# Performance work log

Hardware: AMD Instinct MI355X
Metric: run time of the kernel (lower is better)

The kernel has to match this reference:

```python
import jax, jax.numpy as jnp
import numpy as np

KERNEL_SIZE = 9
B, C, H, W = 8, 32, 512, 512


def setup_inputs() -> dict:
    key = jax.random.key(0)
    image = jax.random.uniform(key, (B, C, H, W), dtype=jnp.float32)
    return {"image": image}


def _make_kernels(channels, k, dtype):
    # kernel1: point-select (identity) depthwise kernel
    k1 = jnp.zeros((channels, 1, k, k), dtype=dtype).at[:, 0, k // 2, k // 2].set(1.0)
    # kernel2: all -2, center = k*k - 2
    k2 = jnp.full((channels, 1, k, k), -2.0, dtype=dtype).at[:, 0, k // 2, k // 2].set(float(k * k - 2))
    # kernel3: ones box filter
    k3 = jnp.ones((channels, 1, k, k), dtype=dtype)
    return k1, k2, k3


def _dwconv(x, ker, channels, k):
    pad = k // 2  # 'same' padding for odd k
    return jax.lax.conv_general_dilated(
        x, ker,
        window_strides=(1, 1),
        padding=[(pad, pad), (pad, pad)],
        dimension_numbers=("NCHW", "OIHW", "NCHW"),
        feature_group_count=channels,
    )


def reference(image):
    channels = image.shape[1]
    k = KERNEL_SIZE
    k1, k2, k3 = _make_kernels(channels, k, image.dtype)
    im_sq = jnp.square(image)
    conv1 = _dwconv(image, k1, channels, k)   # identity point-select
    conv2 = _dwconv(image, k2, channels, k)   # box(-2) with center correction
    conv3 = _dwconv(im_sq, k3, channels, k)   # box sum of squares
    convsum = conv1 * conv2 + conv3
    # sum over (C,H,W) per batch element, then mean over batch
    return jnp.mean(jnp.sum(convsum, axis=(1, 2, 3)))
```

## Files before the change

kernel.cpp:

```cpp
#include <hip/hip_runtime.h>

#define HH 512
#define WW 512
#define SEGS 16
#define SEGROWS 32
#define CG 128

__device__ __forceinline__ int imax(int a, int b) { return a > b ? a : b; }
__device__ __forceinline__ int imin(int a, int b) { return a < b ? a : b; }

__global__ __launch_bounds__(256, 4) void scc_kernel(const float* __restrict__ img,
                                                     float* __restrict__ out) {
    const int tid   = blockIdx.x * 256 + threadIdx.x;
    const int g     = tid & (CG - 1);
    const int rest  = tid >> 7;
    const int seg   = rest & (SEGS - 1);
    const int plane = rest >> 4;

    const float* base = img + (size_t)plane * (HH * WW);
    const int r0 = seg * SEGROWS;

    float4 cw;
    {
        int w0 = 4 * g;
        cw.x = (float)(9 - imax(0, 4 - (w0 + 0)) - imax(0, (w0 + 0) - (WW - 5)));
        cw.y = (float)(9 - imax(0, 4 - (w0 + 1)) - imax(0, (w0 + 1) - (WW - 5)));
        cw.z = (float)(9 - imax(0, 4 - (w0 + 2)) - imax(0, (w0 + 2) - (WW - 5)));
        cw.w = (float)(9 - imax(0, 4 - (w0 + 3)) - imax(0, (w0 + 3) - (WW - 5)));
    }

    const int offL = imax(g - 1, 0) * 16;
    const int offC = g * 16;
    const int offR = imin(g + 1, CG - 1) * 16;
    const float mL = (g > 0) ? 1.f : 0.f;
    const float mR = (g < CG - 1) ? 1.f : 0.f;

    const float4 z4 = make_float4(0.f, 0.f, 0.f, 0.f);
    float4 x0 = z4, x1 = z4, x2 = z4, x3 = z4, x4 = z4,
           x5 = z4, x6 = z4, x7 = z4, x8 = z4;
    float4 q0 = z4, q1 = z4, q2 = z4, q3 = z4, q4 = z4;
    float4 V = z4;
    float accW = 0.f, accRV = 0.f;

#pragma unroll 8
    for (int i = 0; i < SEGROWS + 8; ++i) {
        const int r  = r0 - 4 + i;
        const int rc_ = imin(imax(r, 0), HH - 1);
        const float m = ((unsigned)r < (unsigned)HH) ? 1.f : 0.f;
        const char* rowb = (const char*)(base + (ptrdiff_t)rc_ * WW);

        float4 lcr = *(const float4*)(rowb + offL);
        float4 ccr = *(const float4*)(rowb + offC);
        float4 rcr = *(const float4*)(rowb + offR);

        const float a = mL * m, b = mR * m;
        float4 lc = make_float4(lcr.x * a, lcr.y * a, lcr.z * a, lcr.w * a);
        float4 cc = make_float4(ccr.x * m, ccr.y * m, ccr.z * m, ccr.w * m);
        float4 rc = make_float4(rcr.x * b, rcr.y * b, rcr.z * b, rcr.w * b);

        float R0 = ((lc.x + lc.y) + (lc.z + lc.w)) + ((cc.x + cc.y) + (cc.z + cc.w)) + rc.x;
        float R1 = R0 - lc.x + rc.y;
        float R2 = R1 - lc.y + rc.z;
        float R3 = R2 - lc.z + rc.w;
        float4 Rn = make_float4(R0, R1, R2, R3);

        V.x += cc.x - x0.x;  V.y += cc.y - x0.y;
        V.z += cc.z - x0.z;  V.w += cc.w - x0.w;

        x0 = x1; x1 = x2; x2 = x3; x3 = x4; x4 = x5;
        x5 = x6; x6 = x7; x7 = x8; x8 = cc;
        q0 = q1; q1 = q2; q2 = q3; q3 = q4; q4 = Rn;

        if (i >= 8) {
            const int h = r - 4;
            const float chf = (float)(9 - imax(0, 4 - h) - imax(0, h - (HH - 5)));
            float w0 = fmaf(chf, cw.x, 81.f);
            float w1 = fmaf(chf, cw.y, 81.f);
            float w2 = fmaf(chf, cw.z, 81.f);
            float w3 = fmaf(chf, cw.w, 81.f);
            accW = fmaf(w0 * x4.x, x4.x, accW);
            accW = fmaf(w1 * x4.y, x4.y, accW);
            accW = fmaf(w2 * x4.z, x4.z, accW);
            accW = fmaf(w3 * x4.w, x4.w, accW);
            accRV = fmaf(q0.x, V.x, accRV);
            accRV = fmaf(q0.y, V.y, accRV);
            accRV = fmaf(q0.z, V.z, accRV);
            accRV = fmaf(q0.w, V.w, accRV);
        }
    }

    float acc = accW - 2.f * accRV;

#pragma unroll
    for (int off = 32; off > 0; off >>= 1)
        acc += __shfl_xor(acc, off, 64);
    __shared__ float wsum[4];
    const int lane = threadIdx.x & 63;
    const int wv   = threadIdx.x >> 6;
    if (lane == 0) wsum[wv] = acc;
    __syncthreads();
    if (threadIdx.x == 0) {
        float s = (wsum[0] + wsum[1]) + (wsum[2] + wsum[3]);
        atomicAdd(out, 0.125f * s);
    }
}

extern "C" void kernel_launch(void* const* d_in, const int* in_sizes, int n_in,
                              void* d_out, int out_size, void* d_ws, size_t ws_size,
                              hipStream_t stream) {
    const float* img = (const float*)d_in[0];
    float* out = (float*)d_out;
    hipMemsetAsync(out, 0, sizeof(float), stream);
    scc_kernel<<<dim3(2048), dim3(256), 0, stream>>>(img, out);
}
```

Baseline: 370.6 us.

## Replace register row history with cache reloads and peel warm-up loop

The nine-row float4 register history used for the vertical sliding sum is removed. The row leaving the window and the center row are now reloaded from memory, expected to hit in cache. The first eight warm-up rows are peeled into their own loop, which drops the per-iteration branch, and the launch-bounds occupancy hint is removed. This lowers register pressure and may improve occupancy, at the cost of two extra float4 loads per row.

```diff
diff --git a/kernel.cpp b/kernel.cpp
--- a/kernel.cpp
+++ b/kernel.cpp
@@ -9,8 +9,8 @@
 __device__ __forceinline__ int imax(int a, int b) { return a > b ? a : b; }
 __device__ __forceinline__ int imin(int a, int b) { return a < b ? a : b; }
 
-__global__ __launch_bounds__(256, 4) void scc_kernel(const float* __restrict__ img,
-                                                     float* __restrict__ out) {
+__global__ __launch_bounds__(256) void scc_kernel(const float* __restrict__ img,
+                                                  float* __restrict__ out) {
     const int tid   = blockIdx.x * 256 + threadIdx.x;
     const int g     = tid & (CG - 1);
     const int rest  = tid >> 7;
@@ -36,57 +36,76 @@
     const float mR = (g < CG - 1) ? 1.f : 0.f;
 
     const float4 z4 = make_float4(0.f, 0.f, 0.f, 0.f);
-    float4 x0 = z4, x1 = z4, x2 = z4, x3 = z4, x4 = z4,
-           x5 = z4, x6 = z4, x7 = z4, x8 = z4;
     float4 q0 = z4, q1 = z4, q2 = z4, q3 = z4, q4 = z4;
     float4 V = z4;
     float accW = 0.f, accRV = 0.f;
 
-#pragma unroll 8
-    for (int i = 0; i < SEGROWS + 8; ++i) {
-        const int r  = r0 - 4 + i;
-        const int rc_ = imin(imax(r, 0), HH - 1);
-        const float m = ((unsigned)r < (unsigned)HH) ? 1.f : 0.f;
-        const char* rowb = (const char*)(base + (ptrdiff_t)rc_ * WW);
+#pragma unroll
+    for (int i = 0; i < 8; ++i) {
+        const int r   = r0 - 4 + i;
+        const int rcl = imax(r, 0);
+        const float m = (r >= 0) ? 1.f : 0.f;
+        const char* rowb = (const char*)(base + (ptrdiff_t)rcl * WW);
+        float4 L = *(const float4*)(rowb + offL);
+        float4 C = *(const float4*)(rowb + offC);
+        float4 Rv = *(const float4*)(rowb + offR);
+        const float a = mL * m, b = mR * m;
+        float4 lc = make_float4(L.x * a, L.y * a, L.z * a, L.w * a);
+        float4 cc = make_float4(C.x * m, C.y * m, C.z * m, C.w * m);
+        float4 rc = make_float4(Rv.x * b, Rv.y * b, Rv.z * b, Rv.w * b);
+        float R0 = ((lc.x + lc.y) + (lc.z + lc.w)) + ((cc.x + cc.y) + (cc.z + cc.w)) + rc.x;
+        float R1 = R0 - lc.x + rc.y;
+        float R2 = R1 - lc.y + rc.z;
+        float R3 = R2 - lc.z + rc.w;
+        V.x += cc.x; V.y += cc.y; V.z += cc.z; V.w += cc.w;
+        q0 = q1; q1 = q2; q2 = q3; q3 = q4; q4 = make_float4(R0, R1, R2, R3);
+    }
 
-        float4 lcr = *(const float4*)(rowb + offL);
-        float4 ccr = *(const float4*)(rowb + offC);
-        float4 rcr = *(const float4*)(rowb + offR);
+#pragma unroll 4
+    for (int i = 8; i < SEGROWS + 8; ++i) {
+        const int r   = r0 - 4 + i;
+        const int rcl = imin(r, HH - 1);
+        const float m = (r < HH) ? 1.f : 0.f;
+        const int rm9 = r - 9;
+        const int r9c = imax(rm9, 0);
+        const float ms = (i >= 9 && rm9 >= 0) ? 1.f : 0.f;
+        const int h = r - 4;
+
+        const char* rowb = (const char*)(base + (ptrdiff_t)rcl * WW);
+        float4 L  = *(const float4*)(rowb + offL);
+        float4 C  = *(const float4*)(rowb + offC);
+        float4 Rv = *(const float4*)(rowb + offR);
+        float4 C9 = *(const float4*)((const char*)(base + (ptrdiff_t)r9c * WW) + offC);
+        float4 Ch = *(const float4*)((const char*)(base + (ptrdiff_t)h   * WW) + offC);
 
         const float a = mL * m, b = mR * m;
-        float4 lc = make_float4(lcr.x * a, lcr.y * a, lcr.z * a, lcr.w * a);
-        float4 cc = make_float4(ccr.x * m, ccr.y * m, ccr.z * m, ccr.w * m);
-        float4 rc = make_float4(rcr.x * b, rcr.y * b, rcr.z * b, rcr.w * b);
+        float4 lc = make_float4(L.x * a, L.y * a, L.z * a, L.w * a);
+        float4 cc = make_float4(C.x * m, C.y * m, C.z * m, C.w * m);
+        float4 rc = make_float4(Rv.x * b, Rv.y * b, Rv.z * b, Rv.w * b);
 
         float R0 = ((lc.x + lc.y) + (lc.z + lc.w)) + ((cc.x + cc.y) + (cc.z + cc.w)) + rc.x;
         float R1 = R0 - lc.x + rc.y;
         float R2 = R1 - lc.y + rc.z;
         float R3 = R2 - lc.z + rc.w;
-        float4 Rn = make_float4(R0, R1, R2, R3);
 
-        V.x += cc.x - x0.x;  V.y += cc.y - x0.y;
-        V.z += cc.z - x0.z;  V.w += cc.w - x0.w;
+        V.x += cc.x - C9.x * ms;  V.y += cc.y - C9.y * ms;
+        V.z += cc.z - C9.z * ms;  V.w += cc.w - C9.w * ms;
 
-        x0 = x1; x1 = x2; x2 = x3; x3 = x4; x4 = x5;
-        x5 = x6; x6 = x7; x7 = x8; x8 = cc;
-        q0 = q1; q1 = q2; q2 = q3; q3 = q4; q4 = Rn;
+        q0 = q1; q1 = q2; q2 = q3; q3 = q4; q4 = make_float4(R0, R1, R2, R3);
 
-        if (i >= 8) {
-            const int h = r - 4;
-            const float chf = (float)(9 - imax(0, 4 - h) - imax(0, h - (HH - 5)));
-            float w0 = fmaf(chf, cw.x, 81.f);
-            float w1 = fmaf(chf, cw.y, 81.f);
-            float w2 = fmaf(chf, cw.z, 81.f);
-            float w3 = fmaf(chf, cw.w, 81.f);
-            accW = fmaf(w0 * x4.x, x4.x, accW);
-            accW = fmaf(w1 * x4.y, x4.y, accW);
-            accW = fmaf(w2 * x4.z, x4.z, accW);
-            accW = fmaf(w3 * x4.w, x4.w, accW);
-            accRV = fmaf(q0.x, V.x, accRV);
-            accRV = fmaf(q0.y, V.y, accRV);
-            accRV = fmaf(q0.z, V.z, accRV);
-            accRV = fmaf(q0.w, V.w, accRV);
-        }
+        const float chf = (float)(9 - imax(0, 4 - h) - imax(0, h - (HH - 5)));
+        float w0 = fmaf(chf, cw.x, 81.f);
+        float w1 = fmaf(chf, cw.y, 81.f);
+        float w2 = fmaf(chf, cw.z, 81.f);
+        float w3 = fmaf(chf, cw.w, 81.f);
+        accW = fmaf(w0 * Ch.x, Ch.x, accW);
+        accW = fmaf(w1 * Ch.y, Ch.y, accW);
+        accW = fmaf(w2 * Ch.z, Ch.z, accW);
+        accW = fmaf(w3 * Ch.w, Ch.w, accW);
+        accRV = fmaf(q0.x, V.x, accRV);
+        accRV = fmaf(q0.y, V.y, accRV);
+        accRV = fmaf(q0.z, V.z, accRV);
+        accRV = fmaf(q0.w, V.w, accRV);
     }
 
     float acc = accW - 2.f * accRV;
```

Result: slower. 397.4 us (+7.2%).
